# Kernel optimization log

Hardware: AMD Instinct MI355X
Metric: run time of the kernel (lower is better)

The kernel has to match this reference:

```python
import jax, jax.numpy as jnp
import numpy as np

B, FEAT, SFEAT, N, E = 64, 512, 128, 10000, 160000


def setup_inputs() -> dict:
    key = jax.random.key(0)
    ks = jax.random.split(key, 8)
    net = jax.random.normal(ks[0], (B, FEAT + SFEAT), dtype=jnp.float32)
    edge_index = jax.random.randint(ks[1], (2, E), 0, N, dtype=jnp.int64)
    s = 0.02
    return {
        "net": net,
        "edge_index": edge_index,
        "W_mlp2": jax.random.normal(ks[2], (FEAT + SFEAT, 2 * FEAT), dtype=jnp.float32) * s,
        "W_logr": jax.random.normal(ks[3], (FEAT, N * 3), dtype=jnp.float32) * s,
        "W_s": jax.random.normal(ks[4], (FEAT, N * 6), dtype=jnp.float32) * s,
        "W1_logr": jax.random.normal(ks[5], (3, 3), dtype=jnp.float32) * 0.3,
        "b1_logr": jnp.zeros((3,), jnp.float32),
        "W1_s": jax.random.normal(ks[6], (6, 6), dtype=jnp.float32) * 0.3,
        "b1_s": jnp.zeros((6,), jnp.float32),
        "W4_s": jax.random.normal(ks[7], (6, 6), dtype=jnp.float32) * 0.3,
        "b4_s": jnp.zeros((6,), jnp.float32),
    }


def gcn(x, src, dst, W, b):
    # GCNConv with added self-loops and symmetric normalization.
    # x: [B, N, C_in]; src/dst: [E+N] (self-loops pre-appended by caller)
    n = x.shape[1]
    deg = jax.ops.segment_sum(jnp.ones_like(dst, dtype=x.dtype), dst, num_segments=n)
    dinv = jnp.where(deg > 0, jax.lax.rsqrt(deg), 0.0)
    norm = dinv[src] * dinv[dst]  # [E+N]
    h = jnp.einsum("bnc,cd->bnd", x, W)  # transform first (C small)
    msg = h[:, src, :] * norm[None, :, None]  # gather + scale
    out = jnp.zeros_like(h).at[:, dst].add(msg)  # scatter-add over nodes
    return out + b


def reference(net, edge_index, W_mlp2, W_logr, W_s, W1_logr, b1_logr, W1_s, b1_s, W4_s, b4_s):
    loop = jnp.arange(N, dtype=edge_index.dtype)
    src = jnp.concatenate([edge_index[0], loop])
    dst = jnp.concatenate([edge_index[1], loop])

    net = jnp.tanh(net @ W_mlp2)  # [B, 2*FEAT]
    net_logr = jnp.tanh((net[:, :FEAT] @ W_logr).reshape(-1, N, 3))
    net_s = jnp.tanh((net[:, FEAT:2 * FEAT] @ W_s).reshape(-1, N, 6))

    net_logr = gcn(net_logr, src, dst, W1_logr, b1_logr)
    net_s = jnp.tanh(gcn(net_s, src, dst, W1_s, b1_s))
    net_s = gcn(net_s, src, dst, W4_s, b4_s)

    return jnp.concatenate([net_logr * 4.0, net_s * 50.0], axis=2)  # [B, N, 9]
```

## Files before the change

kernel.cpp:

```cpp
#include <hip/hip_runtime.h>
#include <math.h>

#define NNODE 10000
#define NEDGE 160000
#define BATCH 64
#define KDIM  512

__device__ __forceinline__ unsigned short f2bf(float x) {
  union { float f; unsigned u; } v; v.f = x;
  return (unsigned short)((v.u + 0x7FFF + ((v.u >> 16) & 1)) >> 16);
}
__device__ __forceinline__ float bf2f(unsigned short h) {
  union { unsigned u; float f; } v; v.u = ((unsigned)h) << 16;
  return v.f;
}


__global__ void k_init_counts(int* counts) {
  int i = blockIdx.x * 256 + threadIdx.x;
  if (i < NNODE) counts[i] = 1;
}

__global__ void k_count(const int* __restrict__ ei, int* counts) {
  int e = blockIdx.x * 256 + threadIdx.x;
  if (e < NEDGE) atomicAdd(&counts[ei[NEDGE + e]], 1);
}

__global__ __launch_bounds__(1024) void k_scan(const int* __restrict__ counts,
                                               int* offs, int* cursor, float* dinv) {
  __shared__ int sd[1024];
  int t = threadIdx.x;
  int b0 = t * 10, b1 = b0 + 10;
  if (b1 > NNODE) b1 = NNODE;
  if (b0 > NNODE) b0 = NNODE;
  int s = 0;
  for (int i = b0; i < b1; i++) s += counts[i];
  sd[t] = s;
  __syncthreads();
  for (int off = 1; off < 1024; off <<= 1) {
    int v = (t >= off) ? sd[t - off] : 0;
    __syncthreads();
    sd[t] += v;
    __syncthreads();
  }
  int excl = (t == 0) ? 0 : sd[t - 1];
  for (int i = b0; i < b1; i++) {
    offs[i] = excl;
    cursor[i] = excl;
    dinv[i] = rsqrtf((float)counts[i]);
    excl += counts[i];
  }
  if (t == 1023) offs[NNODE] = sd[1023];
}

__global__ void k_fill(const int* __restrict__ ei, const float* __restrict__ dinv,
                       int* cursor, int* srcn, float* wnorm) {
  int e = blockIdx.x * 256 + threadIdx.x;
  if (e >= NEDGE + NNODE) return;
  int s, d;
  if (e < NEDGE) { s = ei[e]; d = ei[NEDGE + e]; }
  else           { s = e - NEDGE; d = s; }
  int pos = atomicAdd(&cursor[d], 1);
  srcn[pos] = s;
  wnorm[pos] = dinv[s] * dinv[d];
}


__global__ __launch_bounds__(256) void k_mlp2(const float* __restrict__ net,
                                              const float* __restrict__ W,
                                              float* __restrict__ net1) {
  __shared__ float a[640];
  int bb = blockIdx.x >> 2, cg = (blockIdx.x & 3) << 8;
  int t = threadIdx.x;
  for (int i = t; i < 640; i += 256) a[i] = net[bb * 640 + i];
  __syncthreads();
  float acc = 0.f;
#pragma unroll 4
  for (int k = 0; k < 640; k++) acc += a[k] * W[k * 1024 + cg + t];
  net1[bb * 1024 + cg + t] = tanhf(acc);
}


template <int C>
__device__ __forceinline__ void gemm_body(const float* __restrict__ A,
                                          const float* __restrict__ W,
                                          const float* __restrict__ W1,
                                          float* lds, float* w1sh,
                                          unsigned short* __restrict__ Hout,
                                          int NC, int blk) {
  constexpr int NODE_F = 64 * C;
  constexpr int NODE_P = NODE_F + 4;
  int tid = threadIdx.x;
  if (tid < C * C) w1sh[tid] = W1[tid];
  int tc = tid % 12, tr = tid / 12;
  int c0 = blk * 48;

  float acc[4][4];
#pragma unroll
  for (int i = 0; i < 4; i++)
#pragma unroll
    for (int j = 0; j < 4; j++) acc[i][j] = 0.f;

  for (int kc = 0; kc < KDIM; kc += 64) {
    __syncthreads();
    for (int idx = tid; idx < 64 * 64; idx += 192) {
      int r = idx >> 6, kk = idx & 63;
      lds[r * 68 + kk] = A[r * 1024 + kc + kk];
    }
    __syncthreads();
#pragma unroll 2
    for (int k = 0; k < 64; k += 4) {
      const float* Wp = W + (size_t)(kc + k) * NC + c0 + tc * 4;
      float4 w0 = *(const float4*)(Wp);
      float4 w1 = *(const float4*)(Wp + NC);
      float4 w2 = *(const float4*)(Wp + 2 * (size_t)NC);
      float4 w3 = *(const float4*)(Wp + 3 * (size_t)NC);
#pragma unroll
      for (int i = 0; i < 4; i++) {
        const float4 av = *(const float4*)&lds[(tr + 16 * i) * 68 + k];
        acc[i][0] += av.x * w0.x + av.y * w1.x + av.z * w2.x + av.w * w3.x;
        acc[i][1] += av.x * w0.y + av.y * w1.y + av.z * w2.y + av.w * w3.y;
        acc[i][2] += av.x * w0.z + av.y * w1.z + av.z * w2.z + av.w * w3.z;
        acc[i][3] += av.x * w0.w + av.y * w1.w + av.z * w2.w + av.w * w3.w;
      }
    }
  }
  __syncthreads();

#pragma unroll
  for (int j = 0; j < 4; j++) {
    int cl = tc * 4 + j;
    int nl = cl / C, ccl = cl % C;
    float* lp = lds + nl * NODE_P + ccl;
#pragma unroll
    for (int i = 0; i < 4; i++) {
      int b = tr + 16 * i;
      lp[b * C] = tanhf(acc[i][j]);
    }
  }
  __syncthreads();

  unsigned short* Hb = Hout + (size_t)c0 * 64;
  for (int f = tid * 4; f < 48 * 64; f += 192 * 4) {
    float vals[4];
#pragma unroll
    for (int e = 0; e < 4; e++) {
      int idx = f + e;
      int n = idx / NODE_F, rem = idx - n * NODE_F;
      int b = rem / C, d = rem - b * C;
      const float* row = lds + n * NODE_P + b * C;
      float v = 0.f;
#pragma unroll
      for (int c = 0; c < C; c++) v += row[c] * w1sh[c * C + d];
      vals[e] = v;
    }
    ushort4 o;
    o.x = f2bf(vals[0]); o.y = f2bf(vals[1]);
    o.z = f2bf(vals[2]); o.w = f2bf(vals[3]);
    *(ushort4*)&Hb[f] = o;
  }
}

__global__ __launch_bounds__(192) void k_gemm_both(const float* __restrict__ net1,
                                                   const float* __restrict__ W_logr,
                                                   const float* __restrict__ W_s,
                                                   const float* __restrict__ W1_logr,
                                                   const float* __restrict__ W1_s,
                                                   unsigned short* __restrict__ hA,
                                                   unsigned short* __restrict__ hB) {
  extern __shared__ float lds[];
  __shared__ float w1sh[36];
  int blk = blockIdx.x;
  if (blk < 1250) gemm_body<6>(net1 + 512, W_s, W1_s, lds, w1sh, hB, 60000, blk);
  else            gemm_body<3>(net1, W_logr, W1_logr, lds, w1sh, hA, 30000, blk - 1250);
}


template <int C>
__global__ __launch_bounds__(64 * C) void k_gather_out(const unsigned short* __restrict__ h,
    const int* __restrict__ offs, const int* __restrict__ srcn,
    const float* __restrict__ wn, const float* __restrict__ bias,
    float* __restrict__ out, float scale, int outc0) {
  constexpr int BC = 64 * C;
  int n = blockIdx.x, t = threadIdx.x;
  int beg = offs[n], end = offs[n + 1];
  float acc = 0.f;
  int k = beg;
  for (; k + 2 <= end; k += 2) {
    int s0 = srcn[k], s1 = srcn[k + 1];
    float w0 = wn[k], w1 = wn[k + 1];
    acc += w0 * bf2f(h[(size_t)s0 * BC + t]);
    acc += w1 * bf2f(h[(size_t)s1 * BC + t]);
  }
  if (k < end) acc += wn[k] * bf2f(h[(size_t)srcn[k] * BC + t]);
  int b = t / C, c = t - b * C;
  out[(size_t)b * (NNODE * 9) + n * 9 + outc0 + c] = (acc + bias[c]) * scale;
}

__global__ __launch_bounds__(384) void k_gather_mid(const unsigned short* __restrict__ h,
    const int* __restrict__ offs, const int* __restrict__ srcn,
    const float* __restrict__ wn, const float* __restrict__ b1,
    const float* __restrict__ W4, unsigned short* __restrict__ hC) {
  __shared__ float sd[384];
  __shared__ float w4[36];
  int n = blockIdx.x, t = threadIdx.x;
  if (t < 36) w4[t] = W4[t];
  int beg = offs[n], end = offs[n + 1];
  float acc = 0.f;
  int k = beg;
  for (; k + 2 <= end; k += 2) {
    int s0 = srcn[k], s1 = srcn[k + 1];
    float w0 = wn[k], w1 = wn[k + 1];
    acc += w0 * bf2f(h[(size_t)s0 * 384 + t]);
    acc += w1 * bf2f(h[(size_t)s1 * 384 + t]);
  }
  if (k < end) acc += wn[k] * bf2f(h[(size_t)srcn[k] * 384 + t]);
  int b = t / 6, c = t - b * 6;
  sd[t] = tanhf(acc + b1[c]);
  __syncthreads();
  float o = 0.f;
#pragma unroll
  for (int c2 = 0; c2 < 6; c2++) o += sd[b * 6 + c2] * w4[c2 * 6 + c];
  hC[(size_t)n * 384 + t] = f2bf(o);
}


extern "C" void kernel_launch(void* const* d_in, const int* in_sizes, int n_in,
                              void* d_out, int out_size, void* d_ws, size_t ws_size,
                              hipStream_t stream) {
  const float* net     = (const float*)d_in[0];
  const int*   ei      = (const int*)d_in[1];
  const float* W_mlp2  = (const float*)d_in[2];
  const float* W_logr  = (const float*)d_in[3];
  const float* W_s     = (const float*)d_in[4];
  const float* W1_logr = (const float*)d_in[5];
  const float* b1_logr = (const float*)d_in[6];
  const float* W1_s    = (const float*)d_in[7];
  const float* b1_s    = (const float*)d_in[8];
  const float* W4_s    = (const float*)d_in[9];
  const float* b4_s    = (const float*)d_in[10];
  float* out = (float*)d_out;

  char* w = (char*)d_ws;
  auto carve = [&](size_t nbytes) {
    char* p = w;
    w += (nbytes + 255) & ~(size_t)255;
    return p;
  };
  int*            counts = (int*)           carve(NNODE * 4);
  int*            offs   = (int*)           carve((NNODE + 1) * 4);
  int*            cursor = (int*)           carve(NNODE * 4);
  float*          dinv   = (float*)         carve(NNODE * 4);
  int*            srcn   = (int*)           carve((NEDGE + NNODE) * 4);
  float*          wnorm  = (float*)         carve((NEDGE + NNODE) * 4);
  float*          net1   = (float*)         carve(BATCH * 1024 * 4);
  unsigned short* hA     = (unsigned short*)carve((size_t)NNODE * BATCH * 3 * 2);
  unsigned short* hB     = (unsigned short*)carve((size_t)NNODE * BATCH * 6 * 2);
  unsigned short* hC     = (unsigned short*)carve((size_t)NNODE * BATCH * 6 * 2);

  k_init_counts<<<(NNODE + 255) / 256, 256, 0, stream>>>(counts);
  k_count<<<(NEDGE + 255) / 256, 256, 0, stream>>>(ei, counts);
  k_scan<<<1, 1024, 0, stream>>>(counts, offs, cursor, dinv);
  k_fill<<<(NEDGE + NNODE + 255) / 256, 256, 0, stream>>>(ei, dinv, cursor, srcn, wnorm);

  k_mlp2<<<256, 256, 0, stream>>>(net, W_mlp2, net1);
  k_gemm_both<<<1875, 192, 17408, stream>>>(net1, W_logr, W_s, W1_logr, W1_s, hA, hB);

  k_gather_out<3><<<NNODE, 192, 0, stream>>>(hA, offs, srcn, wnorm, b1_logr, out, 4.0f, 0);

  k_gather_mid<<<NNODE, 384, 0, stream>>>(hB, offs, srcn, wnorm, b1_s, W4_s, hC);
  k_gather_out<6><<<NNODE, 384, 0, stream>>>(hC, offs, srcn, wnorm, b4_s, out, 50.0f, 3);
}
```

Baseline: 713.2 us.

## Widen GEMM tiles, drop LDS A staging, fuse output gathers, swizzle node order

The GEMM now gives each thread 8 columns (96 per block, about half as many blocks) and reads A straight from global memory instead of staging it in LDS. The final-tile edge case is handled by clamping the column base and masking writes. The two output gather kernels are merged into one 576-thread kernel that writes all 9 channels per node. The gather kernels process 4 edges per step and visit nodes in a swizzled order, and the mlp2 unroll goes from 4 to 8. The aims are fewer launches, more independent loads in flight and better output write coalescing, at the cost of more registers in the GEMM and repeated global reads of A.

```diff
diff --git a/kernel.cpp b/kernel.cpp
--- a/kernel.cpp
+++ b/kernel.cpp
@@ -75,7 +75,7 @@
   for (int i = t; i < 640; i += 256) a[i] = net[bb * 640 + i];
   __syncthreads();
   float acc = 0.f;
-#pragma unroll 4
+#pragma unroll 8
   for (int k = 0; k < 640; k++) acc += a[k] * W[k * 1024 + cg + t];
   net1[bb * 1024 + cg + t] = tanhf(acc);
 }
@@ -93,55 +93,64 @@
   int tid = threadIdx.x;
   if (tid < C * C) w1sh[tid] = W1[tid];
   int tc = tid % 12, tr = tid / 12;
-  int c0 = blk * 48;
-
-  float acc[4][4];
+  int c0 = blk * 96;
+  int cb = min(c0 + tc * 8, NC - 8);
+
+  float acc[4][8];
 #pragma unroll
   for (int i = 0; i < 4; i++)
 #pragma unroll
-    for (int j = 0; j < 4; j++) acc[i][j] = 0.f;
-
-  for (int kc = 0; kc < KDIM; kc += 64) {
-    __syncthreads();
-    for (int idx = tid; idx < 64 * 64; idx += 192) {
-      int r = idx >> 6, kk = idx & 63;
-      lds[r * 68 + kk] = A[r * 1024 + kc + kk];
-    }
-    __syncthreads();
+    for (int j = 0; j < 8; j++) acc[i][j] = 0.f;
+
 #pragma unroll 2
-    for (int k = 0; k < 64; k += 4) {
-      const float* Wp = W + (size_t)(kc + k) * NC + c0 + tc * 4;
-      float4 w0 = *(const float4*)(Wp);
-      float4 w1 = *(const float4*)(Wp + NC);
-      float4 w2 = *(const float4*)(Wp + 2 * (size_t)NC);
-      float4 w3 = *(const float4*)(Wp + 3 * (size_t)NC);
+  for (int k = 0; k < KDIM; k += 4) {
+    float4 av[4];
+#pragma unroll
+    for (int i = 0; i < 4; i++)
+      av[i] = *(const float4*)&A[(tr + 16 * i) * 1024 + k];
+    const float* Wp = W + (size_t)k * NC + cb;
+    float4 wv[4][2];
+#pragma unroll
+    for (int kk = 0; kk < 4; kk++) {
+      wv[kk][0] = *(const float4*)(Wp + (size_t)kk * NC);
+      wv[kk][1] = *(const float4*)(Wp + (size_t)kk * NC + 4);
+    }
+#pragma unroll
+    for (int i = 0; i < 4; i++) {
+#pragma unroll
+      for (int jh = 0; jh < 2; jh++) {
+        acc[i][jh * 4 + 0] += av[i].x * wv[0][jh].x + av[i].y * wv[1][jh].x +
+                              av[i].z * wv[2][jh].x + av[i].w * wv[3][jh].x;
+        acc[i][jh * 4 + 1] += av[i].x * wv[0][jh].y + av[i].y * wv[1][jh].y +
+                              av[i].z * wv[2][jh].y + av[i].w * wv[3][jh].y;
+        acc[i][jh * 4 + 2] += av[i].x * wv[0][jh].z + av[i].y * wv[1][jh].z +
+                              av[i].z * wv[2][jh].z + av[i].w * wv[3][jh].z;
+        acc[i][jh * 4 + 3] += av[i].x * wv[0][jh].w + av[i].y * wv[1][jh].w +
+                              av[i].z * wv[2][jh].w + av[i].w * wv[3][jh].w;
+      }
+    }
+  }
+
+  int nact = min(96, NC - c0);
+  __syncthreads();
+#pragma unroll
+  for (int j = 0; j < 8; j++) {
+    int cl = tc * 8 + j;
+    if (cl < nact) {
+      int nl = cl / C, ccl = cl % C;
+      float* lp = lds + nl * NODE_P + ccl;
 #pragma unroll
       for (int i = 0; i < 4; i++) {
-        const float4 av = *(const float4*)&lds[(tr + 16 * i) * 68 + k];
-        acc[i][0] += av.x * w0.x + av.y * w1.x + av.z * w2.x + av.w * w3.x;
-        acc[i][1] += av.x * w0.y + av.y * w1.y + av.z * w2.y + av.w * w3.y;
-        acc[i][2] += av.x * w0.z + av.y * w1.z + av.z * w2.z + av.w * w3.z;
-        acc[i][3] += av.x * w0.w + av.y * w1.w + av.z * w2.w + av.w * w3.w;
+        int b = tr + 16 * i;
+        lp[b * C] = tanhf(acc[i][j]);
       }
     }
   }
   __syncthreads();
 
-#pragma unroll
-  for (int j = 0; j < 4; j++) {
-    int cl = tc * 4 + j;
-    int nl = cl / C, ccl = cl % C;
-    float* lp = lds + nl * NODE_P + ccl;
-#pragma unroll
-    for (int i = 0; i < 4; i++) {
-      int b = tr + 16 * i;
-      lp[b * C] = tanhf(acc[i][j]);
-    }
-  }
-  __syncthreads();
-
+  int region = nact * 64;
   unsigned short* Hb = Hout + (size_t)c0 * 64;
-  for (int f = tid * 4; f < 48 * 64; f += 192 * 4) {
+  for (int f = tid * 4; f < region; f += 192 * 4) {
     float vals[4];
 #pragma unroll
     for (int e = 0; e < 4; e++) {
@@ -171,30 +180,12 @@
   extern __shared__ float lds[];
   __shared__ float w1sh[36];
   int blk = blockIdx.x;
-  if (blk < 1250) gemm_body<6>(net1 + 512, W_s, W1_s, lds, w1sh, hB, 60000, blk);
-  else            gemm_body<3>(net1, W_logr, W1_logr, lds, w1sh, hA, 30000, blk - 1250);
-}
-
-
-template <int C>
-__global__ __launch_bounds__(64 * C) void k_gather_out(const unsigned short* __restrict__ h,
-    const int* __restrict__ offs, const int* __restrict__ srcn,
-    const float* __restrict__ wn, const float* __restrict__ bias,
-    float* __restrict__ out, float scale, int outc0) {
-  constexpr int BC = 64 * C;
-  int n = blockIdx.x, t = threadIdx.x;
-  int beg = offs[n], end = offs[n + 1];
-  float acc = 0.f;
-  int k = beg;
-  for (; k + 2 <= end; k += 2) {
-    int s0 = srcn[k], s1 = srcn[k + 1];
-    float w0 = wn[k], w1 = wn[k + 1];
-    acc += w0 * bf2f(h[(size_t)s0 * BC + t]);
-    acc += w1 * bf2f(h[(size_t)s1 * BC + t]);
-  }
-  if (k < end) acc += wn[k] * bf2f(h[(size_t)srcn[k] * BC + t]);
-  int b = t / C, c = t - b * C;
-  out[(size_t)b * (NNODE * 9) + n * 9 + outc0 + c] = (acc + bias[c]) * scale;
+  if (blk < 625) gemm_body<6>(net1 + 512, W_s, W1_s, lds, w1sh, hB, 60000, blk);
+  else           gemm_body<3>(net1, W_logr, W1_logr, lds, w1sh, hA, 30000, blk - 625);
+}
+
+__device__ __forceinline__ int swz_node(int blk) {
+  return (blk & 7) * 1250 + (blk >> 3);
 }
 
 __global__ __launch_bounds__(384) void k_gather_mid(const unsigned short* __restrict__ h,
@@ -203,18 +194,21 @@
     const float* __restrict__ W4, unsigned short* __restrict__ hC) {
   __shared__ float sd[384];
   __shared__ float w4[36];
-  int n = blockIdx.x, t = threadIdx.x;
+  int n = swz_node(blockIdx.x), t = threadIdx.x;
   if (t < 36) w4[t] = W4[t];
   int beg = offs[n], end = offs[n + 1];
   float acc = 0.f;
   int k = beg;
-  for (; k + 2 <= end; k += 2) {
-    int s0 = srcn[k], s1 = srcn[k + 1];
-    float w0 = wn[k], w1 = wn[k + 1];
-    acc += w0 * bf2f(h[(size_t)s0 * 384 + t]);
-    acc += w1 * bf2f(h[(size_t)s1 * 384 + t]);
-  }
-  if (k < end) acc += wn[k] * bf2f(h[(size_t)srcn[k] * 384 + t]);
+  for (; k + 4 <= end; k += 4) {
+    int s0 = srcn[k], s1 = srcn[k + 1], s2 = srcn[k + 2], s3 = srcn[k + 3];
+    float w0 = wn[k], w1 = wn[k + 1], w2 = wn[k + 2], w3 = wn[k + 3];
+    float h0 = bf2f(h[(size_t)s0 * 384 + t]);
+    float h1 = bf2f(h[(size_t)s1 * 384 + t]);
+    float h2 = bf2f(h[(size_t)s2 * 384 + t]);
+    float h3 = bf2f(h[(size_t)s3 * 384 + t]);
+    acc += w0 * h0 + w1 * h1 + w2 * h2 + w3 * h3;
+  }
+  for (; k < end; k++) acc += wn[k] * bf2f(h[(size_t)srcn[k] * 384 + t]);
   int b = t / 6, c = t - b * 6;
   sd[t] = tanhf(acc + b1[c]);
   __syncthreads();
@@ -222,6 +216,35 @@
 #pragma unroll
   for (int c2 = 0; c2 < 6; c2++) o += sd[b * 6 + c2] * w4[c2 * 6 + c];
   hC[(size_t)n * 384 + t] = f2bf(o);
+}
+
+__global__ __launch_bounds__(576) void k_gather_out9(
+    const unsigned short* __restrict__ hA, const unsigned short* __restrict__ hC,
+    const int* __restrict__ offs, const int* __restrict__ srcn,
+    const float* __restrict__ wn, const float* __restrict__ b_logr,
+    const float* __restrict__ b_s, float* __restrict__ out) {
+  int n = swz_node(blockIdx.x), t = threadIdx.x;
+  int b = t / 9, c = t - b * 9;
+  bool isl = (c < 3);
+  const unsigned short* h = isl ? hA : hC;
+  int stride = isl ? 192 : 384;
+  int off = isl ? (b * 3 + c) : (b * 6 + (c - 3));
+  int beg = offs[n], end = offs[n + 1];
+  float acc = 0.f;
+  int k = beg;
+  for (; k + 4 <= end; k += 4) {
+    int s0 = srcn[k], s1 = srcn[k + 1], s2 = srcn[k + 2], s3 = srcn[k + 3];
+    float w0 = wn[k], w1 = wn[k + 1], w2 = wn[k + 2], w3 = wn[k + 3];
+    float h0 = bf2f(h[(size_t)s0 * stride + off]);
+    float h1 = bf2f(h[(size_t)s1 * stride + off]);
+    float h2 = bf2f(h[(size_t)s2 * stride + off]);
+    float h3 = bf2f(h[(size_t)s3 * stride + off]);
+    acc += w0 * h0 + w1 * h1 + w2 * h2 + w3 * h3;
+  }
+  for (; k < end; k++) acc += wn[k] * bf2f(h[(size_t)srcn[k] * stride + off]);
+  float bias = isl ? b_logr[c] : b_s[c - 3];
+  float scale = isl ? 4.0f : 50.0f;
+  out[(size_t)b * (NNODE * 9) + n * 9 + c] = (acc + bias) * scale;
 }
 
 
@@ -264,10 +287,9 @@
   k_fill<<<(NEDGE + NNODE + 255) / 256, 256, 0, stream>>>(ei, dinv, cursor, srcn, wnorm);
 
   k_mlp2<<<256, 256, 0, stream>>>(net, W_mlp2, net1);
-  k_gemm_both<<<1875, 192, 17408, stream>>>(net1, W_logr, W_s, W1_logr, W1_s, hA, hB);
-
-  k_gather_out<3><<<NNODE, 192, 0, stream>>>(hA, offs, srcn, wnorm, b1_logr, out, 4.0f, 0);
+  k_gemm_both<<<938, 192, 25088, stream>>>(net1, W_logr, W_s, W1_logr, W1_s, hA, hB);
 
   k_gather_mid<<<NNODE, 384, 0, stream>>>(hB, offs, srcn, wnorm, b1_s, W4_s, hC);
-  k_gather_out<6><<<NNODE, 384, 0, stream>>>(hC, offs, srcn, wnorm, b4_s, out, 50.0f, 3);
-}
+
+  k_gather_out9<<<NNODE, 576, 0, stream>>>(hA, hC, offs, srcn, wnorm, b1_logr, b4_s, out);
+}
```

After: 575.2 us. 19.4% less time.
